# Optimization experiments

Hardware: AMD Instinct MI355X
Metric: run time of the kernel (lower is better)

## Reference

```python
import jax, jax.numpy as jnp
import numpy as np

B, S, D, H, DFF = 4, 2048, 1024, 16, 4096
DK = D // H
EPS = 1e-5


def setup_inputs() -> dict:
    key = jax.random.key(0)
    ks = jax.random.split(key, 10)
    s = 0.02
    return {
        "x": jax.random.normal(ks[0], (B, S, D), jnp.float32),
        "wq": jax.random.normal(ks[1], (D, D), jnp.float32) * s,
        "wk": jax.random.normal(ks[2], (D, D), jnp.float32) * s,
        "wv": jax.random.normal(ks[3], (D, D), jnp.float32) * s,
        "wo": jax.random.normal(ks[4], (D, D), jnp.float32) * s,
        "w1": jax.random.normal(ks[5], (D, DFF), jnp.float32) * s,
        "b1": jnp.zeros((DFF,), jnp.float32),
        "w2": jax.random.normal(ks[6], (DFF, D), jnp.float32) * s,
        "b2": jnp.zeros((D,), jnp.float32),
        "g1": jnp.ones((D,), jnp.float32),
        "be1": jnp.zeros((D,), jnp.float32),
        "g2": jnp.ones((D,), jnp.float32),
        "be2": jnp.zeros((D,), jnp.float32),
    }


def _layernorm(x, g, b):
    mu = jnp.mean(x, axis=-1, keepdims=True)
    var = jnp.mean(jnp.square(x - mu), axis=-1, keepdims=True)
    return (x - mu) * jax.lax.rsqrt(var + EPS) * g + b


def reference(x, wq, wk, wv, wo, w1, b1, w2, b2, g1, be1, g2, be2):
    # --- self-attention block (pre-LN) ---
    residual = x
    h = _layernorm(x, g1, be1)
    q = (h @ wq).reshape(B, S, H, DK).transpose(0, 2, 1, 3)  # [B,H,S,DK]
    k = (h @ wk).reshape(B, S, H, DK).transpose(0, 2, 1, 3)
    v = (h @ wv).reshape(B, S, H, DK).transpose(0, 2, 1, 3)
    scores = jnp.einsum("bhqd,bhkd->bhqk", q, k) / jnp.sqrt(jnp.float32(DK))
    weights = jax.nn.softmax(scores, axis=-1)
    weights = jnp.nan_to_num(weights, nan=0.0)
    attn = jnp.einsum("bhqk,bhkd->bhqd", weights, v)
    attn = attn.transpose(0, 2, 1, 3).reshape(B, S, D)
    x = residual + attn @ wo
    # --- FFN block (pre-LN) ---
    residual = x
    h = _layernorm(x, g2, be2)
    h = jax.nn.relu(h @ w1 + b1) @ w2 + b2
    return residual + h
```

## Files before the change

### kernel.cpp

```cpp
#include <hip/hip_runtime.h>
#include <stdint.h>

#define B_ 4
#define S_ 2048
#define D_ 1024
#define H_ 16
#define DFF_ 4096
#define QSTR 3072

typedef __attribute__((ext_vector_type(8))) short short8;
typedef __attribute__((ext_vector_type(4))) short short4v;
typedef __attribute__((ext_vector_type(4))) float floatx4;

typedef const __attribute__((address_space(1))) void* gas_ptr;
typedef __attribute__((address_space(3))) void* las_ptr;

__device__ __forceinline__ short f2bf(float f) {
  union { float f; uint32_t u; } v; v.f = f;
  uint32_t r = v.u + 0x7fffu + ((v.u >> 16) & 1u);
  return (short)(r >> 16);
}

__global__ __launch_bounds__(256) void ln_kernel(
    const float* __restrict__ x, const float* __restrict__ g,
    const float* __restrict__ be, short* __restrict__ out)
{
  const int row = blockIdx.x;
  const int tid = threadIdx.x;
  const float4 v = ((const float4*)(x + (size_t)row * D_))[tid];
  float s1 = v.x + v.y + v.z + v.w;
  float s2 = v.x*v.x + v.y*v.y + v.z*v.z + v.w*v.w;
#pragma unroll
  for (int off = 1; off < 64; off <<= 1) {
    s1 += __shfl_xor(s1, off);
    s2 += __shfl_xor(s2, off);
  }
  __shared__ float r1[4], r2[4];
  if ((tid & 63) == 0) { r1[tid >> 6] = s1; r2[tid >> 6] = s2; }
  __syncthreads();
  s1 = r1[0] + r1[1] + r1[2] + r1[3];
  s2 = r2[0] + r2[1] + r2[2] + r2[3];
  const float mu = s1 * (1.0f / D_);
  const float var = s2 * (1.0f / D_) - mu * mu;
  const float rs = rsqrtf(var + 1e-5f);
  const float4 gv = ((const float4*)g)[tid];
  const float4 bv = ((const float4*)be)[tid];
  short4v o;
  o.x = f2bf((v.x - mu) * rs * gv.x + bv.x);
  o.y = f2bf((v.y - mu) * rs * gv.y + bv.y);
  o.z = f2bf((v.z - mu) * rs * gv.z + bv.z);
  o.w = f2bf((v.w - mu) * rs * gv.w + bv.w);
  *(short4v*)&out[(size_t)row * D_ + tid * 4] = o;
}

__global__ __launch_bounds__(256) void transpose_all(
    const float* __restrict__ wq, const float* __restrict__ wk,
    const float* __restrict__ wv, const float* __restrict__ wo,
    const float* __restrict__ w1, const float* __restrict__ w2,
    short* __restrict__ wqkvT, short* __restrict__ woT,
    short* __restrict__ w1T, short* __restrict__ w2T)
{
  const uint32_t pid = blockIdx.x;
  const float* in; short* out;
  int R, C, tile, xsh;
  if (pid < 4096) {
    const int which = pid >> 10; tile = pid & 1023;
    R = 1024; C = 1024; xsh = 5;
    in  = (which == 0) ? wq : (which == 1) ? wk : (which == 2) ? wv : wo;
    out = (which == 3) ? woT : wqkvT + (size_t)which * 1024 * 1024;
  } else if (pid < 8192) {
    tile = pid - 4096; R = 1024; C = 4096; xsh = 7; in = w1; out = w1T;
  } else {
    tile = pid - 8192; R = 4096; C = 1024; xsh = 5; in = w2; out = w2T;
  }
  const int c0 = (tile & ((1 << xsh) - 1)) * 32;
  const int r0 = (tile >> xsh) * 32;

  __shared__ float t[32][33];
  const int tx = threadIdx.x & 31, ty = threadIdx.x >> 5;
#pragma unroll
  for (int i = 0; i < 4; i++)
    t[ty + i * 8][tx] = in[(size_t)(r0 + ty + i * 8) * C + c0 + tx];
  __syncthreads();
#pragma unroll
  for (int i = 0; i < 4; i++)
    out[(size_t)(c0 + ty + i * 8) * R + r0 + tx] = f2bf(t[tx][ty + i * 8]);
}

__global__ __launch_bounds__(256, 4) void gemm_bt(
    const short* __restrict__ A, const short* __restrict__ Bt,
    float* __restrict__ outf, short* __restrict__ outb,
    short* __restrict__ outbK, short* __restrict__ vtT,
    const float* __restrict__ bias, const float* __restrict__ resid,
    int M, int N, int K, int do_relu, int split, int group)
{
  __shared__ short As[2 * 128 * 32];
  __shared__ short Bs[2 * 128 * 32];
  const int tid = threadIdx.x;
  const int wave = tid >> 6;
  const int lane = tid & 63;
  const int quad = lane >> 4;
  const int l16 = lane & 15;

  const uint32_t nblk = gridDim.x;
  const uint32_t pid = blockIdx.y * nblk + blockIdx.x;
  const uint32_t nig = (uint32_t)group * nblk;
  const uint32_t gid = pid / nig;
  const uint32_t within = pid - gid * nig;
  const uint32_t bm = gid * group + within % group;
  const uint32_t bn = within / group;
  const int tm = bm * 128;
  const int tn = bn * 128;

  const int wm = (wave & 1) * 64;
  const int wn = (wave >> 1) * 64;
  const int srow = lane >> 2;
  const int scol = (lane & 3) * 8;

  floatx4 acc[4][4];
#pragma unroll
  for (int i = 0; i < 4; i++)
#pragma unroll
    for (int j = 0; j < 4; j++) acc[i][j] = floatx4{0.f, 0.f, 0.f, 0.f};

  const short* gA0 = A + (size_t)(tm + wave * 32 + srow) * K + scol;
  const short* gB0 = Bt + (size_t)(tn + wave * 32 + srow) * K + scol;

  for (int kt = 0; kt < K; kt += 64) {
    __syncthreads();
    __builtin_amdgcn_global_load_lds((gas_ptr)(gA0 + kt),                      (las_ptr)(&As[wave * 1024]),        16, 0, 0);
    __builtin_amdgcn_global_load_lds((gas_ptr)(gA0 + kt + (size_t)16 * K),     (las_ptr)(&As[wave * 1024 + 512]),  16, 0, 0);
    __builtin_amdgcn_global_load_lds((gas_ptr)(gB0 + kt),                      (las_ptr)(&Bs[wave * 1024]),        16, 0, 0);
    __builtin_amdgcn_global_load_lds((gas_ptr)(gB0 + kt + (size_t)16 * K),     (las_ptr)(&Bs[wave * 1024 + 512]),  16, 0, 0);
    __builtin_amdgcn_global_load_lds((gas_ptr)(gA0 + kt + 32),                 (las_ptr)(&As[4096 + wave * 1024]),       16, 0, 0);
    __builtin_amdgcn_global_load_lds((gas_ptr)(gA0 + kt + 32 + (size_t)16 * K),(las_ptr)(&As[4096 + wave * 1024 + 512]), 16, 0, 0);
    __builtin_amdgcn_global_load_lds((gas_ptr)(gB0 + kt + 32),                 (las_ptr)(&Bs[4096 + wave * 1024]),       16, 0, 0);
    __builtin_amdgcn_global_load_lds((gas_ptr)(gB0 + kt + 32 + (size_t)16 * K),(las_ptr)(&Bs[4096 + wave * 1024 + 512]), 16, 0, 0);
    __syncthreads();

#pragma unroll
    for (int ksub = 0; ksub < 2; ksub++) {
      const int hb = ksub * 4096;
      short8 af[4], bfv[4];
#pragma unroll
      for (int mi = 0; mi < 4; mi++)
        af[mi] = *(const short8*)&As[hb + (wm + mi * 16 + l16) * 32 + quad * 8];
#pragma unroll
      for (int ni = 0; ni < 4; ni++)
        bfv[ni] = *(const short8*)&Bs[hb + (wn + ni * 16 + l16) * 32 + quad * 8];
#pragma unroll
      for (int mi = 0; mi < 4; mi++)
#pragma unroll
        for (int ni = 0; ni < 4; ni++)
          acc[mi][ni] = __builtin_amdgcn_mfma_f32_16x16x32_bf16(af[mi], bfv[ni], acc[mi][ni], 0, 0, 0);
    }
  }

  short* ob = outb;
  int Nst = N;
  int cbase = tn;
  int vpart = 0;
  if (split) {
    const int part = tn >> 10;
    if (part == 2) vpart = 1;
    else ob = (part == 0) ? outb : outbK;
    Nst = D_;
    cbase = tn & (D_ - 1);
  }

  if (vpart) {
#pragma unroll
    for (int mi = 0; mi < 4; mi++) {
      const int row0 = tm + wm + mi * 16 + quad * 4;
      const int bb = row0 >> 11, s0r = row0 & 2047;
#pragma unroll
      for (int ni = 0; ni < 4; ni++) {
        const int cst = cbase + wn + ni * 16 + l16;
        short4v o;
#pragma unroll
        for (int r = 0; r < 4; r++) o[r] = f2bf(acc[mi][ni][r]);
        *(short4v*)&vtT[((size_t)(bb << 10) + cst) * (size_t)S_ + s0r] = o;
      }
    }
    return;
  }

#pragma unroll
  for (int mi = 0; mi < 4; mi++) {
    const int row0 = tm + wm + mi * 16 + quad * 4;
#pragma unroll
    for (int ni = 0; ni < 4; ni++) {
      const int col = tn + wn + ni * 16 + l16;
      const int cst = cbase + wn + ni * 16 + l16;
      const float bv = bias ? bias[col] : 0.0f;
#pragma unroll
      for (int r = 0; r < 4; r++) {
        const size_t idx = (size_t)(row0 + r) * Nst + cst;
        float v = acc[mi][ni][r] + bv;
        if (do_relu) v = fmaxf(v, 0.0f);
        if (resid) v += resid[idx];
        if (outf) outf[idx] = v;
        if (ob) ob[idx] = f2bf(v);
      }
    }
  }
}

__global__ __launch_bounds__(256, 4) void gemm_bt_n64(
    const short* __restrict__ A, const short* __restrict__ Bt,
    float* __restrict__ outf,
    const float* __restrict__ bias, const float* __restrict__ resid,
    int M, int N, int K, int group)
{
  __shared__ short As[2 * 128 * 32];
  __shared__ short Bs[2 * 64 * 32];
  const int tid = threadIdx.x;
  const int wave = tid >> 6;
  const int lane = tid & 63;
  const int quad = lane >> 4;
  const int l16 = lane & 15;

  const uint32_t nblk = gridDim.x;
  const uint32_t pid = blockIdx.y * nblk + blockIdx.x;
  const uint32_t nig = (uint32_t)group * nblk;
  const uint32_t gid = pid / nig;
  const uint32_t within = pid - gid * nig;
  const uint32_t bm = gid * group + within % group;
  const uint32_t bn = within / group;
  const int tm = bm * 128;
  const int tn = bn * 64;

  const int wm = (wave & 1) * 64;
  const int wn = (wave >> 1) * 32;
  const int srow = lane >> 2;
  const int scol = (lane & 3) * 8;

  floatx4 acc[4][2];
#pragma unroll
  for (int i = 0; i < 4; i++)
#pragma unroll
    for (int j = 0; j < 2; j++) acc[i][j] = floatx4{0.f, 0.f, 0.f, 0.f};

  const short* gA0 = A + (size_t)(tm + wave * 32 + srow) * K + scol;
  const short* gB0 = Bt + (size_t)(tn + wave * 16 + srow) * K + scol;

  for (int kt = 0; kt < K; kt += 64) {
    __syncthreads();
    __builtin_amdgcn_global_load_lds((gas_ptr)(gA0 + kt),                      (las_ptr)(&As[wave * 1024]),        16, 0, 0);
    __builtin_amdgcn_global_load_lds((gas_ptr)(gA0 + kt + (size_t)16 * K),     (las_ptr)(&As[wave * 1024 + 512]),  16, 0, 0);
    __builtin_amdgcn_global_load_lds((gas_ptr)(gA0 + kt + 32),                 (las_ptr)(&As[4096 + wave * 1024]),       16, 0, 0);
    __builtin_amdgcn_global_load_lds((gas_ptr)(gA0 + kt + 32 + (size_t)16 * K),(las_ptr)(&As[4096 + wave * 1024 + 512]), 16, 0, 0);
    __builtin_amdgcn_global_load_lds((gas_ptr)(gB0 + kt),      (las_ptr)(&Bs[wave * 512]),        16, 0, 0);
    __builtin_amdgcn_global_load_lds((gas_ptr)(gB0 + kt + 32), (las_ptr)(&Bs[2048 + wave * 512]), 16, 0, 0);
    __syncthreads();

#pragma unroll
    for (int ksub = 0; ksub < 2; ksub++) {
      const int ha = ksub * 4096;
      const int hbv = ksub * 2048;
      short8 af[4], bfv[2];
#pragma unroll
      for (int mi = 0; mi < 4; mi++)
        af[mi] = *(const short8*)&As[ha + (wm + mi * 16 + l16) * 32 + quad * 8];
#pragma unroll
      for (int ni = 0; ni < 2; ni++)
        bfv[ni] = *(const short8*)&Bs[hbv + (wn + ni * 16 + l16) * 32 + quad * 8];
#pragma unroll
      for (int mi = 0; mi < 4; mi++)
#pragma unroll
        for (int ni = 0; ni < 2; ni++)
          acc[mi][ni] = __builtin_amdgcn_mfma_f32_16x16x32_bf16(af[mi], bfv[ni], acc[mi][ni], 0, 0, 0);
    }
  }

#pragma unroll
  for (int mi = 0; mi < 4; mi++) {
    const int row0 = tm + wm + mi * 16 + quad * 4;
#pragma unroll
    for (int ni = 0; ni < 2; ni++) {
      const int col = tn + wn + ni * 16 + l16;
      const float bv = bias ? bias[col] : 0.0f;
#pragma unroll
      for (int r = 0; r < 4; r++) {
        const size_t idx = (size_t)(row0 + r) * N + col;
        float v = acc[mi][ni][r] + bv;
        if (resid) v += resid[idx];
        outf[idx] = v;
      }
    }
  }
}

#define LSTR 68
__global__ __launch_bounds__(256) void attn_kernel(
    const short* __restrict__ qb, const short* __restrict__ kb,
    const short* __restrict__ vtb, short* __restrict__ attb)
{
  __shared__ short Ks[64 * LSTR];
  __shared__ short Vts[64 * LSTR];
  __shared__ short Ps[128 * LSTR];

  const int tid = threadIdx.x;
  const int wave = tid >> 6, lane = tid & 63, quad = lane >> 4, l16 = lane & 15;
  const int qt = blockIdx.x, bh = blockIdx.y;
  const int b = bh >> 4, h = bh & 15;
  const size_t rowbase = (size_t)b * S_;
  const int hcol = h * 64;
  const int r = tid >> 2, c = (tid & 3) * 16;

  short8 qa[2][2];
#pragma unroll
  for (int qs = 0; qs < 2; qs++) {
    const short* gq = qb + (rowbase + qt * 128 + qs * 64 + wave * 16 + l16) * D_ + hcol + quad * 8;
    short8 t0 = *(const short8*)gq;
    short8 t1 = *(const short8*)(gq + 32);
#pragma unroll
    for (int i = 0; i < 8; i++) {
      const float f0 = __uint_as_float(((uint32_t)(uint16_t)t0[i]) << 16) * 0.18033688f;
      const float f1 = __uint_as_float(((uint32_t)(uint16_t)t1[i]) << 16) * 0.18033688f;
      t0[i] = (short)((__float_as_uint(f0) + 0x8000u) >> 16);
      t1[i] = (short)((__float_as_uint(f1) + 0x8000u) >> 16);
    }
    qa[qs][0] = t0;
    qa[qs][1] = t1;
  }

  float l_run[2][4];
  floatx4 Of[2][4];
#pragma unroll
  for (int qs = 0; qs < 2; qs++)
#pragma unroll
    for (int rr = 0; rr < 4; rr++) { l_run[qs][rr] = 0.f; }
#pragma unroll
  for (int qs = 0; qs < 2; qs++)
#pragma unroll
    for (int nd = 0; nd < 4; nd++) Of[qs][nd] = floatx4{0.f, 0.f, 0.f, 0.f};

  const short* gk0 = kb + (rowbase + r) * D_ + hcol + c;
  const short* gv0 = vtb + ((size_t)bh * 64 + r) * S_ + c;

  short8 kr0 = *(const short8*)gk0, kr1 = *(const short8*)(gk0 + 8);
  short8 vr0 = *(const short8*)gv0, vr1 = *(const short8*)(gv0 + 8);

  for (int kt = 0; kt < S_; kt += 64) {
    __syncthreads();
    *(short8*)&Ks[r * LSTR + c]      = kr0;
    *(short8*)&Ks[r * LSTR + c + 8]  = kr1;
    *(short8*)&Vts[r * LSTR + c]     = vr0;
    *(short8*)&Vts[r * LSTR + c + 8] = vr1;
    __syncthreads();

    {
      const int ktn = (kt + 64 < S_) ? kt + 64 : 0;
      const short* gk = gk0 + (size_t)ktn * D_;
      const short* gv = gv0 + ktn;
      kr0 = *(const short8*)gk; kr1 = *(const short8*)(gk + 8);
      vr0 = *(const short8*)gv; vr1 = *(const short8*)(gv + 8);
    }

#pragma unroll
    for (int nk = 0; nk < 4; nk++) {
      const short8 kf0 = *(const short8*)&Ks[(nk * 16 + l16) * LSTR + quad * 8];
      const short8 kf1 = *(const short8*)&Ks[(nk * 16 + l16) * LSTR + 32 + quad * 8];
#pragma unroll
      for (int qs = 0; qs < 2; qs++) {
        floatx4 s = floatx4{0.f, 0.f, 0.f, 0.f};
        s = __builtin_amdgcn_mfma_f32_16x16x32_bf16(qa[qs][0], kf0, s, 0, 0, 0);
        s = __builtin_amdgcn_mfma_f32_16x16x32_bf16(qa[qs][1], kf1, s, 0, 0, 0);
#pragma unroll
        for (int rr = 0; rr < 4; rr++) {
          const float p = __builtin_amdgcn_exp2f(s[rr]);
          l_run[qs][rr] += p;
          Ps[(qs * 64 + wave * 16 + quad * 4 + rr) * LSTR + nk * 16 + l16] =
              (short)((__float_as_uint(p) + 0x8000u) >> 16);
        }
      }
    }

    asm volatile("" ::: "memory");
    short8 pa[2][2];
#pragma unroll
    for (int qs = 0; qs < 2; qs++) {
      pa[qs][0] = *(const short8*)&Ps[(qs * 64 + wave * 16 + l16) * LSTR + quad * 8];
      pa[qs][1] = *(const short8*)&Ps[(qs * 64 + wave * 16 + l16) * LSTR + 32 + quad * 8];
    }
#pragma unroll
    for (int nd = 0; nd < 4; nd++) {
      const short8 vf0 = *(const short8*)&Vts[(nd * 16 + l16) * LSTR + quad * 8];
      const short8 vf1 = *(const short8*)&Vts[(nd * 16 + l16) * LSTR + 32 + quad * 8];
#pragma unroll
      for (int qs = 0; qs < 2; qs++) {
        Of[qs][nd] = __builtin_amdgcn_mfma_f32_16x16x32_bf16(pa[qs][0], vf0, Of[qs][nd], 0, 0, 0);
        Of[qs][nd] = __builtin_amdgcn_mfma_f32_16x16x32_bf16(pa[qs][1], vf1, Of[qs][nd], 0, 0, 0);
      }
    }
  }

#pragma unroll
  for (int off = 1; off < 16; off <<= 1)
#pragma unroll
    for (int qs = 0; qs < 2; qs++)
#pragma unroll
      for (int rr = 0; rr < 4; rr++) l_run[qs][rr] += __shfl_xor(l_run[qs][rr], off);
#pragma unroll
  for (int qs = 0; qs < 2; qs++) {
    float inv[4];
#pragma unroll
    for (int rr = 0; rr < 4; rr++) inv[rr] = 1.0f / l_run[qs][rr];
#pragma unroll
    for (int nd = 0; nd < 4; nd++)
#pragma unroll
      for (int rr = 0; rr < 4; rr++) {
        const int qrow = qt * 128 + qs * 64 + wave * 16 + quad * 4 + rr;
        const int col = hcol + nd * 16 + l16;
        attb[(rowbase + qrow) * D_ + col] = f2bf(Of[qs][nd][rr] * inv[rr]);
      }
  }
}

extern "C" void kernel_launch(void* const* d_in, const int* in_sizes, int n_in,
                              void* d_out, int out_size, void* d_ws, size_t ws_size,
                              hipStream_t stream) {
  const float* x   = (const float*)d_in[0];
  const float* wq  = (const float*)d_in[1];
  const float* wk  = (const float*)d_in[2];
  const float* wv  = (const float*)d_in[3];
  const float* wo  = (const float*)d_in[4];
  const float* w1  = (const float*)d_in[5];
  const float* b1  = (const float*)d_in[6];
  const float* w2  = (const float*)d_in[7];
  const float* b2  = (const float*)d_in[8];
  const float* g1  = (const float*)d_in[9];
  const float* be1 = (const float*)d_in[10];
  const float* g2  = (const float*)d_in[11];
  const float* be2 = (const float*)d_in[12];
  float* out = (float*)d_out;

  const size_t MROWS = (size_t)B_ * S_;
  char* p = (char*)d_ws;
  auto take = [&](size_t bytes) { char* r = p; p += (bytes + 255) & ~(size_t)255; return r; };
  short* hb    = (short*)take(MROWS * D_ * 2);
  short* h2b   = (short*)take(MROWS * D_ * 2);
  short* qbuf  = (short*)take(MROWS * D_ * 2);
  short* kbuf  = (short*)take(MROWS * D_ * 2);
  short* vtb   = (short*)take(MROWS * D_ * 2);
  short* attb  = (short*)take(MROWS * D_ * 2);
  short* ffb   = (short*)take(MROWS * DFF_ * 2);
  short* wqkvT = (short*)take((size_t)3 * D_ * D_ * 2);
  short* woT   = (short*)take((size_t)D_ * D_ * 2);
  short* w1T   = (short*)take((size_t)D_ * DFF_ * 2);
  short* w2T   = (short*)take((size_t)DFF_ * D_ * 2);
  float* x1    = (float*)take(MROWS * D_ * 4);

  transpose_all<<<12288, 256, 0, stream>>>(wq, wk, wv, wo, w1, w2,
                                           wqkvT, woT, w1T, w2T);

  ln_kernel<<<MROWS, 256, 0, stream>>>(x, g1, be1, hb);

  gemm_bt<<<dim3(QSTR / 128, MROWS / 128), 256, 0, stream>>>(
      hb, wqkvT, nullptr, qbuf, kbuf, vtb, nullptr, nullptr, MROWS, QSTR, D_, 0, 1, 8);

  attn_kernel<<<dim3(S_ / 128, B_ * H_), 256, 0, stream>>>(qbuf, kbuf, vtb, attb);

  gemm_bt_n64<<<dim3(D_ / 64, MROWS / 128), 256, 0, stream>>>(
      attb, woT, x1, nullptr, x, MROWS, D_, D_, 8);

  ln_kernel<<<MROWS, 256, 0, stream>>>(x1, g2, be2, h2b);

  gemm_bt<<<dim3(DFF_ / 128, MROWS / 128), 256, 0, stream>>>(
      h2b, w1T, nullptr, ffb, nullptr, nullptr, b1, nullptr, MROWS, DFF_, D_, 1, 0, 8);

  gemm_bt_n64<<<dim3(D_ / 64, MROWS / 128), 256, 0, stream>>>(
      ffb, w2T, out, b2, x1, MROWS, D_, DFF_, 4);

  (void)in_sizes; (void)n_in; (void)out_size; (void)ws_size;
}
```

Measured before the change: 553.8 us.

## Restructure attention with 32x32 MFMA, register-resident P, swizzled double-buffered LDS

Rewrites the attention kernel to use 32x32x16 bf16 MFMA computing S^T (K as the A operand), so that probabilities stay in registers. They are repacked via v_cvt_pk_bf16_f32 and v_permlane32_swap into the A operand of the PV MFMA, removing the P round-trip through shared memory. K/V tiles move to an XOR-swizzled, double-buffered LDS layout with one barrier per iteration, and the launch bounds request more occupancy. This aims to cut LDS traffic, bank conflicts and syncs, at the cost of complex lane mapping that must be exactly right for correctness.

```diff
diff --git a/kernel.cpp b/kernel.cpp
--- a/kernel.cpp
+++ b/kernel.cpp
@@ -11,6 +11,7 @@
 typedef __attribute__((ext_vector_type(8))) short short8;
 typedef __attribute__((ext_vector_type(4))) short short4v;
 typedef __attribute__((ext_vector_type(4))) float floatx4;
+typedef __attribute__((ext_vector_type(16))) float floatx16;
 
 typedef const __attribute__((address_space(1))) void* gas_ptr;
 typedef __attribute__((address_space(3))) void* las_ptr;
@@ -291,130 +292,126 @@
   }
 }
 
-#define LSTR 68
-__global__ __launch_bounds__(256) void attn_kernel(
+__device__ __forceinline__ int kvidx(int row, int scol) {
+  return (row << 6) + (scol ^ ((row & 7) << 3));
+}
+
+__global__ __launch_bounds__(256, 4) void attn_kernel(
     const short* __restrict__ qb, const short* __restrict__ kb,
     const short* __restrict__ vtb, short* __restrict__ attb)
 {
-  __shared__ short Ks[64 * LSTR];
-  __shared__ short Vts[64 * LSTR];
-  __shared__ short Ps[128 * LSTR];
+  __shared__ short Ks[2][64 * 64];
+  __shared__ short Vts[2][64 * 64];
+  __shared__ float lbuf[4][32];
 
   const int tid = threadIdx.x;
-  const int wave = tid >> 6, lane = tid & 63, quad = lane >> 4, l16 = lane & 15;
+  const int wave = tid >> 6, lane = tid & 63;
+  const int l31 = lane & 31, hi = lane >> 5;
   const int qt = blockIdx.x, bh = blockIdx.y;
   const int b = bh >> 4, h = bh & 15;
   const size_t rowbase = (size_t)b * S_;
   const int hcol = h * 64;
   const int r = tid >> 2, c = (tid & 3) * 16;
 
-  short8 qa[2][2];
-#pragma unroll
-  for (int qs = 0; qs < 2; qs++) {
-    const short* gq = qb + (rowbase + qt * 128 + qs * 64 + wave * 16 + l16) * D_ + hcol + quad * 8;
-    short8 t0 = *(const short8*)gq;
-    short8 t1 = *(const short8*)(gq + 32);
-#pragma unroll
-    for (int i = 0; i < 8; i++) {
-      const float f0 = __uint_as_float(((uint32_t)(uint16_t)t0[i]) << 16) * 0.18033688f;
-      const float f1 = __uint_as_float(((uint32_t)(uint16_t)t1[i]) << 16) * 0.18033688f;
-      t0[i] = (short)((__float_as_uint(f0) + 0x8000u) >> 16);
-      t1[i] = (short)((__float_as_uint(f1) + 0x8000u) >> 16);
-    }
-    qa[qs][0] = t0;
-    qa[qs][1] = t1;
-  }
-
-  float l_run[2][4];
-  floatx4 Of[2][4];
-#pragma unroll
-  for (int qs = 0; qs < 2; qs++)
-#pragma unroll
-    for (int rr = 0; rr < 4; rr++) { l_run[qs][rr] = 0.f; }
-#pragma unroll
-  for (int qs = 0; qs < 2; qs++)
-#pragma unroll
-    for (int nd = 0; nd < 4; nd++) Of[qs][nd] = floatx4{0.f, 0.f, 0.f, 0.f};
+  short8 qf[4];
+  {
+    const short* gq = qb + (rowbase + qt * 128 + wave * 32 + l31) * D_ + hcol + hi * 8;
+#pragma unroll
+    for (int st = 0; st < 4; st++) {
+      short8 t = *(const short8*)(gq + st * 16);
+#pragma unroll
+      for (int i = 0; i < 8; i++) {
+        const float f = __uint_as_float(((uint32_t)(uint16_t)t[i]) << 16) * 0.18033688f;
+        t[i] = (short)((__float_as_uint(f) + 0x8000u) >> 16);
+      }
+      qf[st] = t;
+    }
+  }
+
+  floatx16 Of[2];
+#pragma unroll
+  for (int nd = 0; nd < 2; nd++)
+#pragma unroll
+    for (int i = 0; i < 16; i++) Of[nd][i] = 0.f;
+  float lrun = 0.f;
 
   const short* gk0 = kb + (rowbase + r) * D_ + hcol + c;
   const short* gv0 = vtb + ((size_t)bh * 64 + r) * S_ + c;
 
   short8 kr0 = *(const short8*)gk0, kr1 = *(const short8*)(gk0 + 8);
   short8 vr0 = *(const short8*)gv0, vr1 = *(const short8*)(gv0 + 8);
+  *(short8*)&Ks[0][kvidx(r, c)]      = kr0;
+  *(short8*)&Ks[0][kvidx(r, c + 8)]  = kr1;
+  *(short8*)&Vts[0][kvidx(r, c)]     = vr0;
+  *(short8*)&Vts[0][kvidx(r, c + 8)] = vr1;
 
   for (int kt = 0; kt < S_; kt += 64) {
-    __syncthreads();
-    *(short8*)&Ks[r * LSTR + c]      = kr0;
-    *(short8*)&Ks[r * LSTR + c + 8]  = kr1;
-    *(short8*)&Vts[r * LSTR + c]     = vr0;
-    *(short8*)&Vts[r * LSTR + c + 8] = vr1;
-    __syncthreads();
-
-    {
-      const int ktn = (kt + 64 < S_) ? kt + 64 : 0;
-      const short* gk = gk0 + (size_t)ktn * D_;
-      const short* gv = gv0 + ktn;
+    const int cur = (kt >> 6) & 1;
+    const bool more = (kt + 64 < S_);
+    if (more) {
+      const short* gk = gk0 + (size_t)(kt + 64) * D_;
+      const short* gv = gv0 + (kt + 64);
       kr0 = *(const short8*)gk; kr1 = *(const short8*)(gk + 8);
       vr0 = *(const short8*)gv; vr1 = *(const short8*)(gv + 8);
     }
-
-#pragma unroll
-    for (int nk = 0; nk < 4; nk++) {
-      const short8 kf0 = *(const short8*)&Ks[(nk * 16 + l16) * LSTR + quad * 8];
-      const short8 kf1 = *(const short8*)&Ks[(nk * 16 + l16) * LSTR + 32 + quad * 8];
-#pragma unroll
-      for (int qs = 0; qs < 2; qs++) {
-        floatx4 s = floatx4{0.f, 0.f, 0.f, 0.f};
-        s = __builtin_amdgcn_mfma_f32_16x16x32_bf16(qa[qs][0], kf0, s, 0, 0, 0);
-        s = __builtin_amdgcn_mfma_f32_16x16x32_bf16(qa[qs][1], kf1, s, 0, 0, 0);
-#pragma unroll
-        for (int rr = 0; rr < 4; rr++) {
-          const float p = __builtin_amdgcn_exp2f(s[rr]);
-          l_run[qs][rr] += p;
-          Ps[(qs * 64 + wave * 16 + quad * 4 + rr) * LSTR + nk * 16 + l16] =
-              (short)((__float_as_uint(p) + 0x8000u) >> 16);
+    __syncthreads();
+
+#pragma unroll
+    for (int sub = 0; sub < 2; sub++) {
+      floatx16 s;
+#pragma unroll
+      for (int i = 0; i < 16; i++) s[i] = 0.f;
+#pragma unroll
+      for (int st = 0; st < 4; st++) {
+        const short8 kf = *(const short8*)&Ks[cur][kvidx(sub * 32 + l31, st * 16 + hi * 8)];
+        s = __builtin_amdgcn_mfma_f32_32x32x16_bf16(kf, qf[st], s, 0, 0, 0);
+      }
+      float p[16];
+#pragma unroll
+      for (int i = 0; i < 16; i++) { p[i] = __builtin_amdgcn_exp2f(s[i]); lrun += p[i]; }
+      short8 pf[2];
+#pragma unroll
+      for (int kw = 0; kw < 2; kw++) {
+        const int o = kw * 8;
+        uint32_t wa, wb, wc, wd;
+        asm("v_cvt_pk_bf16_f32 %0, %1, %2" : "=v"(wa) : "v"(p[o + 0]), "v"(p[o + 1]));
+        asm("v_cvt_pk_bf16_f32 %0, %1, %2" : "=v"(wb) : "v"(p[o + 4]), "v"(p[o + 5]));
+        asm("v_cvt_pk_bf16_f32 %0, %1, %2" : "=v"(wc) : "v"(p[o + 2]), "v"(p[o + 3]));
+        asm("v_cvt_pk_bf16_f32 %0, %1, %2" : "=v"(wd) : "v"(p[o + 6]), "v"(p[o + 7]));
+        asm("v_permlane32_swap_b32 %0, %1" : "+v"(wa), "+v"(wb));
+        asm("v_permlane32_swap_b32 %0, %1" : "+v"(wc), "+v"(wd));
+        union { uint32_t u[4]; short8 s8; } pk;
+        pk.u[0] = wa; pk.u[1] = wc; pk.u[2] = wb; pk.u[3] = wd;
+        pf[kw] = pk.s8;
+      }
+#pragma unroll
+      for (int kw = 0; kw < 2; kw++)
+#pragma unroll
+        for (int nd = 0; nd < 2; nd++) {
+          const short8 vf = *(const short8*)&Vts[cur][kvidx(nd * 32 + l31, sub * 32 + kw * 16 + hi * 8)];
+          Of[nd] = __builtin_amdgcn_mfma_f32_32x32x16_bf16(pf[kw], vf, Of[nd], 0, 0, 0);
         }
-      }
-    }
-
-    asm volatile("" ::: "memory");
-    short8 pa[2][2];
-#pragma unroll
-    for (int qs = 0; qs < 2; qs++) {
-      pa[qs][0] = *(const short8*)&Ps[(qs * 64 + wave * 16 + l16) * LSTR + quad * 8];
-      pa[qs][1] = *(const short8*)&Ps[(qs * 64 + wave * 16 + l16) * LSTR + 32 + quad * 8];
-    }
-#pragma unroll
-    for (int nd = 0; nd < 4; nd++) {
-      const short8 vf0 = *(const short8*)&Vts[(nd * 16 + l16) * LSTR + quad * 8];
-      const short8 vf1 = *(const short8*)&Vts[(nd * 16 + l16) * LSTR + 32 + quad * 8];
-#pragma unroll
-      for (int qs = 0; qs < 2; qs++) {
-        Of[qs][nd] = __builtin_amdgcn_mfma_f32_16x16x32_bf16(pa[qs][0], vf0, Of[qs][nd], 0, 0, 0);
-        Of[qs][nd] = __builtin_amdgcn_mfma_f32_16x16x32_bf16(pa[qs][1], vf1, Of[qs][nd], 0, 0, 0);
-      }
-    }
-  }
-
-#pragma unroll
-  for (int off = 1; off < 16; off <<= 1)
-#pragma unroll
-    for (int qs = 0; qs < 2; qs++)
-#pragma unroll
-      for (int rr = 0; rr < 4; rr++) l_run[qs][rr] += __shfl_xor(l_run[qs][rr], off);
-#pragma unroll
-  for (int qs = 0; qs < 2; qs++) {
-    float inv[4];
-#pragma unroll
-    for (int rr = 0; rr < 4; rr++) inv[rr] = 1.0f / l_run[qs][rr];
-#pragma unroll
-    for (int nd = 0; nd < 4; nd++)
-#pragma unroll
-      for (int rr = 0; rr < 4; rr++) {
-        const int qrow = qt * 128 + qs * 64 + wave * 16 + quad * 4 + rr;
-        const int col = hcol + nd * 16 + l16;
-        attb[(rowbase + qrow) * D_ + col] = f2bf(Of[qs][nd][rr] * inv[rr]);
-      }
+    }
+
+    if (more) {
+      const int nxt = cur ^ 1;
+      *(short8*)&Ks[nxt][kvidx(r, c)]      = kr0;
+      *(short8*)&Ks[nxt][kvidx(r, c + 8)]  = kr1;
+      *(short8*)&Vts[nxt][kvidx(r, c)]     = vr0;
+      *(short8*)&Vts[nxt][kvidx(r, c + 8)] = vr1;
+    }
+  }
+
+  const float ltot = lrun + __shfl_xor(lrun, 32);
+  if (hi == 0) lbuf[wave][l31] = ltot;
+  asm volatile("" ::: "memory");
+#pragma unroll
+  for (int reg = 0; reg < 16; reg++) {
+    const int q = (reg & 3) + 4 * hi + 8 * (reg >> 2);
+    const float inv = 1.0f / lbuf[wave][q];
+    const size_t base = (rowbase + qt * 128 + wave * 32 + q) * D_ + hcol + l31;
+    attb[base]      = f2bf(Of[0][reg] * inv);
+    attb[base + 32] = f2bf(Of[1][reg] * inv);
   }
 }
 
```

Measured after the change: 547.0 us. About the same (-1.2%).
